# Kernel tuning notes

Hardware: AMD Instinct MI355X
Metric: run time of the kernel (lower is better)

Reference implementation:

```python
import jax, jax.numpy as jnp
import numpy as np

D_MODEL = 1024
H = 16
DK = D_MODEL // H


def setup_inputs() -> dict:
    key = jax.random.key(0)
    ks = jax.random.split(key, 13)
    B, S = 2, 2048
    scale = 1.0 / np.sqrt(D_MODEL)
    inp = {
        "query": jax.random.normal(ks[0], (B, S, D_MODEL), jnp.float32),
        "key": jax.random.normal(ks[1], (B, S, D_MODEL), jnp.float32),
        "value": jax.random.normal(ks[2], (B, S, D_MODEL), jnp.float32),
        "mask": jax.random.randint(ks[3], (B, 1, S, S), 0, 2, jnp.int32),
        "Wq": jax.random.normal(ks[4], (D_MODEL, D_MODEL), jnp.float32) * scale,
        "bq": jnp.zeros((D_MODEL,), jnp.float32),
        "Wk": jax.random.normal(ks[5], (D_MODEL, D_MODEL), jnp.float32) * scale,
        "bk": jnp.zeros((D_MODEL,), jnp.float32),
        "Wv": jax.random.normal(ks[6], (D_MODEL, D_MODEL), jnp.float32) * scale,
        "bv": jnp.zeros((D_MODEL,), jnp.float32),
        "Wo": jax.random.normal(ks[7], (D_MODEL, D_MODEL), jnp.float32) * scale,
        "bo": jnp.zeros((D_MODEL,), jnp.float32),
    }
    return inp


def _split_heads(x, W, b):
    # torch Linear: x @ W.T + b; then [B,S,D] -> [B,H,S,DK]
    B, S, _ = x.shape
    out = x @ W.T + b
    return out.reshape(B, S, H, DK).transpose(0, 2, 1, 3)


def reference(query, key, value, mask, Wq, bq, Wk, bk, Wv, bv, Wo, bo):
    B, S, _ = query.shape
    q = _split_heads(query, Wq, bq)   # [B,H,S,DK]
    k = _split_heads(key, Wk, bk)
    v = _split_heads(value, Wv, bv)
    scores = jnp.einsum("bhqd,bhkd->bhqk", q, k) / jnp.sqrt(jnp.asarray(DK, q.dtype))
    scores = jnp.where(mask == 0, jnp.asarray(-1e9, scores.dtype), scores)
    prob = jax.nn.softmax(scores, axis=-1)
    out = jnp.einsum("bhqk,bhkd->bhqd", prob, v)  # [B,H,S,DK]
    out = out.transpose(0, 2, 1, 3).reshape(B, S, D_MODEL)
    return out @ Wo.T + bo
```

## Files before the change

kernel.cpp:

```cpp
#include <hip/hip_runtime.h>
#include <hip/hip_bf16.h>

#define B_   2
#define S_   2048
#define DM   1024
#define NH   16
#define DKH  64
#define Mdim 4096
#define Ndim 1024
#define Kdim 1024

typedef __attribute__((ext_vector_type(8))) short bf16x8;
typedef __attribute__((ext_vector_type(4))) short bf16x4;
typedef __attribute__((ext_vector_type(4))) float f32x4;

__device__ __forceinline__ short f2b(float x) {
  union { __hip_bfloat16 h; short s; } u;
  u.h = __float2bfloat16(x);
  return u.s;
}

__device__ __forceinline__ void async_copy16(const void* g, void* l) {
  __builtin_amdgcn_global_load_lds(
      (const __attribute__((address_space(1))) unsigned int*)g,
      (__attribute__((address_space(3))) unsigned int*)l, 16, 0, 0);
}

struct Cvt7 {
  const float* src[7];
  ushort* dst[7];
  int n[7];
};

__global__ __launch_bounds__(256) void cvt_all(Cvt7 c) {
  const int ten = blockIdx.y;
  const int base = (blockIdx.x * 256 + threadIdx.x) * 8;
  if (base >= c.n[ten]) return;
  const float* s = c.src[ten] + base;
  float4 a = *(const float4*)s;
  float4 b = *(const float4*)(s + 4);
  bf16x8 r;
  r[0] = f2b(a.x); r[1] = f2b(a.y); r[2] = f2b(a.z); r[3] = f2b(a.w);
  r[4] = f2b(b.x); r[5] = f2b(b.y); r[6] = f2b(b.z); r[7] = f2b(b.w);
  *(bf16x8*)(c.dst[ten] + base) = r;
}

__device__ __forceinline__ void gstore(float* C, size_t i, float v) { C[i] = v; }
__device__ __forceinline__ void gstore(ushort* C, size_t i, float v) { C[i] = (ushort)f2b(v); }

template <typename OutT, int VT>
__global__ __launch_bounds__(256) void gemm128(const ushort* __restrict__ A,
                                               const ushort* __restrict__ W,
                                               const float* __restrict__ bias,
                                               OutT* __restrict__ C, float scale) {
  const int t = threadIdx.x;
  const int w = t >> 6, lane = t & 63;
  const int quad = lane >> 4, r16 = lane & 15;
  const int wr = w >> 1, wc = w & 1;
  const int row0 = blockIdx.x * 128, col0 = blockIdx.y * 64;

  __shared__ alignas(16) ushort a_s[128 * 32];
  __shared__ alignas(16) ushort b_s[64 * 32];

  const int sr = lane >> 2, sc = (lane & 3) * 8;
  const ushort* Ag0 = A + (size_t)(row0 + w * 32 + sr) * Kdim + sc;
  const ushort* Ag1 = Ag0 + (size_t)16 * Kdim;
  const ushort* Wg  = W + (size_t)(col0 + w * 16 + sr) * Kdim + sc;
  ushort* al0 = &a_s[(w * 32) * 32];
  ushort* al1 = &a_s[(w * 32 + 16) * 32];
  ushort* bl  = &b_s[(w * 16) * 32];

  f32x4 acc[4][2];
#pragma unroll
  for (int mt = 0; mt < 4; ++mt)
#pragma unroll
    for (int nt = 0; nt < 2; ++nt) acc[mt][nt] = (f32x4){0.f, 0.f, 0.f, 0.f};

  for (int k0 = 0; k0 < Kdim; k0 += 32) {
    __syncthreads();
    async_copy16(Ag0 + k0, al0);
    async_copy16(Ag1 + k0, al1);
    async_copy16(Wg + k0, bl);
    __syncthreads();

    bf16x8 af[4], bfr[2];
#pragma unroll
    for (int mt = 0; mt < 4; ++mt)
      af[mt] = *(const bf16x8*)&a_s[(wr * 64 + mt * 16 + r16) * 32 + quad * 8];
#pragma unroll
    for (int nt = 0; nt < 2; ++nt)
      bfr[nt] = *(const bf16x8*)&b_s[(wc * 32 + nt * 16 + r16) * 32 + quad * 8];
#pragma unroll
    for (int mt = 0; mt < 4; ++mt)
#pragma unroll
      for (int nt = 0; nt < 2; ++nt)
        acc[mt][nt] = __builtin_amdgcn_mfma_f32_16x16x32_bf16(af[mt], bfr[nt],
                                                              acc[mt][nt], 0, 0, 0);
  }

#pragma unroll
  for (int mt = 0; mt < 4; ++mt) {
#pragma unroll
    for (int nt = 0; nt < 2; ++nt) {
      const int col = col0 + wc * 32 + nt * 16 + r16;
      const float bv = bias[col];
      const int rowb = row0 + wr * 64 + mt * 16 + quad * 4;
#pragma unroll
      for (int i = 0; i < 4; ++i) {
        const float v = (acc[mt][nt][i] + bv) * scale;
        if (VT) {
          const int row = rowb + i;
          const int bb = row >> 11, ss = row & (S_ - 1);
          const int hh = col >> 6, dd = col & 63;
          gstore(C, (((size_t)bb * NH + hh) * 64 + dd) * S_ + ss, v);
        } else {
          gstore(C, (size_t)rowb * Ndim + (size_t)i * Ndim + col, v);
        }
      }
    }
  }
}

__global__ __launch_bounds__(256) void attn_mfma(const ushort* __restrict__ Qp,
                                                 const ushort* __restrict__ Kp,
                                                 const ushort* __restrict__ Vt,
                                                 const int* __restrict__ mask,
                                                 ushort* __restrict__ Oa) {
  const int bh = blockIdx.y;
  const int b = bh >> 4, h = bh & 15;
  const int q0 = blockIdx.x * 64;
  const int t = threadIdx.x;
  const int w = t >> 6, lane = t & 63, quad = lane >> 4, r16 = lane & 15;
  const size_t rb = (size_t)b * S_;

  __shared__ alignas(16) ushort k_s[64 * 64];
  __shared__ alignas(16) ushort vt_s[64 * 64];
  __shared__ alignas(16) ushort p_s[4][16 * 76];

  const ushort* qptr = Qp + (rb + q0 + w * 16 + r16) * DM + h * 64 + quad * 8;
  const bf16x8 aq0 = *(const bf16x8*)qptr;
  const bf16x8 aq1 = *(const bf16x8*)(qptr + 32);

  float l_i[4] = {0.f, 0.f, 0.f, 0.f};
  f32x4 oacc[4];
#pragma unroll
  for (int nt = 0; nt < 4; ++nt) oacc[nt] = (f32x4){0.f, 0.f, 0.f, 0.f};

  const int srow = t >> 3, schunk = t & 7;
  const ushort* kbase = Kp + (rb + srow) * DM + h * 64 + schunk * 8;
  const ushort* vbase = Vt + ((size_t)bh * 64 + srow) * S_ + schunk * 8;
  const int srow2 = srow + 32;

  for (int kt = 0; kt < S_; kt += 64) {
    __syncthreads();
    *(bf16x8*)&k_s[srow * 64 + ((schunk ^ (srow & 7)) * 8)] =
        *(const bf16x8*)(kbase + (size_t)kt * DM);
    *(bf16x8*)&k_s[srow2 * 64 + ((schunk ^ (srow2 & 7)) * 8)] =
        *(const bf16x8*)(kbase + (size_t)(kt + 32) * DM);
    *(bf16x8*)&vt_s[srow * 64 + ((schunk ^ (srow & 7)) * 8)] =
        *(const bf16x8*)(vbase + kt);
    *(bf16x8*)&vt_s[srow2 * 64 + ((schunk ^ (srow2 & 7)) * 8)] =
        *(const bf16x8*)(vbase + (size_t)32 * S_ + kt);
    __syncthreads();

    f32x4 sacc[4];
#pragma unroll
    for (int nt = 0; nt < 4; ++nt) {
      sacc[nt] = (f32x4){0.f, 0.f, 0.f, 0.f};
      const int krow = nt * 16 + r16;
      const bf16x8 b0 = *(const bf16x8*)&k_s[krow * 64 + ((quad ^ (krow & 7)) * 8)];
      const bf16x8 b1 = *(const bf16x8*)&k_s[krow * 64 + (((4 + quad) ^ (krow & 7)) * 8)];
      sacc[nt] = __builtin_amdgcn_mfma_f32_16x16x32_bf16(aq0, b0, sacc[nt], 0, 0, 0);
      sacc[nt] = __builtin_amdgcn_mfma_f32_16x16x32_bf16(aq1, b1, sacc[nt], 0, 0, 0);
    }

    const int* mrow = mask + (size_t)b * S_ * S_ +
                      (size_t)(q0 + w * 16 + quad * 4) * S_ + kt;
#pragma unroll
    for (int i = 0; i < 4; ++i) {
      float ps = 0.f;
#pragma unroll
      for (int nt = 0; nt < 4; ++nt) {
        const int mv = mrow[(size_t)i * S_ + nt * 16 + r16];
        const float p = (mv == 0) ? 0.f : __expf(sacc[nt][i]);
        ps += p;
        p_s[w][(quad * 4 + i) * 76 + nt * 16 + r16] = (ushort)f2b(p);
      }
      l_i[i] += ps;
    }

#pragma unroll
    for (int ks = 0; ks < 2; ++ks) {
      const bf16x4 lo = *(const bf16x4*)&p_s[w][r16 * 76 + ks * 32 + quad * 8];
      const bf16x4 hi = *(const bf16x4*)&p_s[w][r16 * 76 + ks * 32 + quad * 8 + 4];
      bf16x8 pa;
#pragma unroll
      for (int j = 0; j < 4; ++j) { pa[j] = lo[j]; pa[4 + j] = hi[j]; }
      const int kc = ks * 4 + quad;
#pragma unroll
      for (int nt = 0; nt < 4; ++nt) {
        const int dk = nt * 16 + r16;
        const bf16x8 vb = *(const bf16x8*)&vt_s[dk * 64 + ((kc ^ (dk & 7)) * 8)];
        oacc[nt] = __builtin_amdgcn_mfma_f32_16x16x32_bf16(pa, vb, oacc[nt], 0, 0, 0);
      }
    }
  }

#pragma unroll
  for (int i = 0; i < 4; ++i) {
    float l = l_i[i];
#pragma unroll
    for (int off = 1; off < 16; off <<= 1) l += __shfl_xor(l, off);
    l_i[i] = l;
  }
#pragma unroll
  for (int nt = 0; nt < 4; ++nt) {
#pragma unroll
    for (int i = 0; i < 4; ++i) {
      const int row = q0 + w * 16 + quad * 4 + i;
      const int col = h * 64 + nt * 16 + r16;
      Oa[(rb + row) * DM + col] = (ushort)f2b(oacc[nt][i] / l_i[i]);
    }
  }
}

extern "C" void kernel_launch(void* const* d_in, const int* in_sizes, int n_in,
                              void* d_out, int out_size, void* d_ws, size_t ws_size,
                              hipStream_t stream) {
  const int* mask = (const int*)d_in[3];
  const float* bq = (const float*)d_in[5];
  const float* bk = (const float*)d_in[7];
  const float* bv = (const float*)d_in[9];
  const float* bo = (const float*)d_in[11];

  const size_t NE = (size_t)B_ * S_ * DM;
  const size_t NW = (size_t)DM * DM;

  ushort* qc = (ushort*)d_ws;
  ushort* kc = qc + NE;
  ushort* vc = kc + NE;
  ushort* Qp = vc + NE;
  ushort* Kp = Qp + NE;
  ushort* Vt = Kp + NE;
  ushort* Wqc = Vt + NE;
  ushort* Wkc = Wqc + NW;
  ushort* Wvc = Wkc + NW;
  ushort* Woc = Wvc + NW;

  Cvt7 c;
  const int sidx[7] = {0, 1, 2, 4, 6, 8, 10};
  ushort* dsts[7] = {qc, kc, vc, Wqc, Wkc, Wvc, Woc};
  for (int i = 0; i < 7; ++i) {
    c.src[i] = (const float*)d_in[sidx[i]];
    c.dst[i] = dsts[i];
    c.n[i] = (i < 3) ? (int)NE : (int)NW;
  }
  cvt_all<<<dim3(2048, 7), 256, 0, stream>>>(c);

  dim3 gg(Mdim / 128, Ndim / 64);
  gemm128<ushort, 0><<<gg, 256, 0, stream>>>(qc, Wqc, bq, Qp, 0.125f);
  gemm128<ushort, 0><<<gg, 256, 0, stream>>>(kc, Wkc, bk, Kp, 1.0f);
  gemm128<ushort, 1><<<gg, 256, 0, stream>>>(vc, Wvc, bv, Vt, 1.0f);

  attn_mfma<<<dim3(S_ / 64, B_ * NH), 256, 0, stream>>>(Qp, Kp, Vt, mask, qc);

  gemm128<float, 0><<<gg, 256, 0, stream>>>(qc, Woc, bo, (float*)d_out, 1.0f);
}
```

Baseline: 291.9 us.

## Pack mask to bitmask, pre-swizzle K/V layouts for async LDS loads, widen GEMM tiles

Adds a kernel that packs the int32 mask into 64-bit ballot bitmasks, so attention reads far fewer mask bytes. The K and V projection GEMMs now write head-major, XOR-swizzled layouts, which lets attention stage K/V tiles with direct global-to-LDS async copies instead of register round trips. GEMM tiles grow from 128x64 to 128x128 to increase reuse. The packed mask is stored in the kc buffer after the K projection has consumed it, which relies on stream ordering.

```diff
diff --git a/kernel.cpp b/kernel.cpp
--- a/kernel.cpp
+++ b/kernel.cpp
@@ -5,9 +5,7 @@
 #define S_   2048
 #define DM   1024
 #define NH   16
-#define DKH  64
 #define Mdim 4096
-#define Ndim 1024
 #define Kdim 1024
 
 typedef __attribute__((ext_vector_type(8))) short bf16x8;
@@ -45,55 +43,64 @@
   *(bf16x8*)(c.dst[ten] + base) = r;
 }
 
-__device__ __forceinline__ void gstore(float* C, size_t i, float v) { C[i] = v; }
-__device__ __forceinline__ void gstore(ushort* C, size_t i, float v) { C[i] = (ushort)f2b(v); }
-
-template <typename OutT, int VT>
-__global__ __launch_bounds__(256) void gemm128(const ushort* __restrict__ A,
-                                               const ushort* __restrict__ W,
-                                               const float* __restrict__ bias,
-                                               OutT* __restrict__ C, float scale) {
+__global__ __launch_bounds__(256) void pack_mask(const int* __restrict__ mask,
+                                                 unsigned long long* __restrict__ mpk) {
+  const int gw = (blockIdx.x * 256 + threadIdx.x) >> 6;
+  const int lane = threadIdx.x & 63;
+  const int mv = mask[(size_t)gw * 64 + lane];
+  const unsigned long long bits = __ballot(mv != 0);
+  if (lane == 0) mpk[gw] = bits;
+}
+
+template <int MODE>
+__global__ __launch_bounds__(256) void gemm_m97(const ushort* __restrict__ A,
+                                                const ushort* __restrict__ W,
+                                                const float* __restrict__ bias,
+                                                void* __restrict__ Cv, float scale) {
   const int t = threadIdx.x;
   const int w = t >> 6, lane = t & 63;
   const int quad = lane >> 4, r16 = lane & 15;
   const int wr = w >> 1, wc = w & 1;
-  const int row0 = blockIdx.x * 128, col0 = blockIdx.y * 64;
+  const int row0 = blockIdx.x * 128, col0 = blockIdx.y * 128;
 
   __shared__ alignas(16) ushort a_s[128 * 32];
-  __shared__ alignas(16) ushort b_s[64 * 32];
-
-  const int sr = lane >> 2, sc = (lane & 3) * 8;
-  const ushort* Ag0 = A + (size_t)(row0 + w * 32 + sr) * Kdim + sc;
-  const ushort* Ag1 = Ag0 + (size_t)16 * Kdim;
-  const ushort* Wg  = W + (size_t)(col0 + w * 16 + sr) * Kdim + sc;
-  ushort* al0 = &a_s[(w * 32) * 32];
-  ushort* al1 = &a_s[(w * 32 + 16) * 32];
-  ushort* bl  = &b_s[(w * 16) * 32];
-
-  f32x4 acc[4][2];
+  __shared__ alignas(16) ushort b_s[128 * 32];
+
+  const int sr = t >> 2, sc = (t & 3) * 8;
+  const ushort* Ag0 = A + (size_t)(row0 + sr) * Kdim + sc;
+  const ushort* Ag1 = Ag0 + (size_t)64 * Kdim;
+  const ushort* Wg0 = W + (size_t)(col0 + sr) * Kdim + sc;
+  const ushort* Wg1 = Wg0 + (size_t)64 * Kdim;
+  ushort* al0 = &a_s[w * 512];
+  ushort* al1 = &a_s[2048 + w * 512];
+  ushort* bl0 = &b_s[w * 512];
+  ushort* bl1 = &b_s[2048 + w * 512];
+
+  f32x4 acc[4][4];
 #pragma unroll
   for (int mt = 0; mt < 4; ++mt)
 #pragma unroll
-    for (int nt = 0; nt < 2; ++nt) acc[mt][nt] = (f32x4){0.f, 0.f, 0.f, 0.f};
+    for (int nt = 0; nt < 4; ++nt) acc[mt][nt] = (f32x4){0.f, 0.f, 0.f, 0.f};
 
   for (int k0 = 0; k0 < Kdim; k0 += 32) {
     __syncthreads();
     async_copy16(Ag0 + k0, al0);
     async_copy16(Ag1 + k0, al1);
-    async_copy16(Wg + k0, bl);
-    __syncthreads();
-
-    bf16x8 af[4], bfr[2];
+    async_copy16(Wg0 + k0, bl0);
+    async_copy16(Wg1 + k0, bl1);
+    __syncthreads();
+
+    bf16x8 af[4], bfr[4];
 #pragma unroll
     for (int mt = 0; mt < 4; ++mt)
       af[mt] = *(const bf16x8*)&a_s[(wr * 64 + mt * 16 + r16) * 32 + quad * 8];
 #pragma unroll
-    for (int nt = 0; nt < 2; ++nt)
-      bfr[nt] = *(const bf16x8*)&b_s[(wc * 32 + nt * 16 + r16) * 32 + quad * 8];
+    for (int nt = 0; nt < 4; ++nt)
+      bfr[nt] = *(const bf16x8*)&b_s[(wc * 64 + nt * 16 + r16) * 32 + quad * 8];
 #pragma unroll
     for (int mt = 0; mt < 4; ++mt)
 #pragma unroll
-      for (int nt = 0; nt < 2; ++nt)
+      for (int nt = 0; nt < 4; ++nt)
         acc[mt][nt] = __builtin_amdgcn_mfma_f32_16x16x32_bf16(af[mt], bfr[nt],
                                                               acc[mt][nt], 0, 0, 0);
   }
@@ -101,20 +108,30 @@
 #pragma unroll
   for (int mt = 0; mt < 4; ++mt) {
 #pragma unroll
-    for (int nt = 0; nt < 2; ++nt) {
-      const int col = col0 + wc * 32 + nt * 16 + r16;
+    for (int nt = 0; nt < 4; ++nt) {
+      const int col = col0 + wc * 64 + nt * 16 + r16;
       const float bv = bias[col];
       const int rowb = row0 + wr * 64 + mt * 16 + quad * 4;
 #pragma unroll
       for (int i = 0; i < 4; ++i) {
         const float v = (acc[mt][nt][i] + bv) * scale;
-        if (VT) {
-          const int row = rowb + i;
-          const int bb = row >> 11, ss = row & (S_ - 1);
-          const int hh = col >> 6, dd = col & 63;
-          gstore(C, (((size_t)bb * NH + hh) * 64 + dd) * S_ + ss, v);
+        const int row = rowb + i;
+        if (MODE == 0) {
+          ((float*)Cv)[(size_t)row * DM + col] = v;
+        } else if (MODE == 1) {
+          ((ushort*)Cv)[(size_t)row * DM + col] = (ushort)f2b(v);
+        } else if (MODE == 2) {
+          const int bb = row >> 11, s = row & (S_ - 1);
+          const int hh = col >> 6, d = col & 63;
+          const size_t idx = ((size_t)(bb * NH + hh) * S_ + s) * 64 +
+                             (((d >> 3) ^ (s & 7)) * 8) + (d & 7);
+          ((ushort*)Cv)[idx] = (ushort)f2b(v);
         } else {
-          gstore(C, (size_t)rowb * Ndim + (size_t)i * Ndim + col, v);
+          const int bb = row >> 11, s = row & (S_ - 1);
+          const int hh = col >> 6, d = col & 63;
+          const size_t idx = ((size_t)(bb * NH + hh) * 64 + d) * S_ + (s & ~63) +
+                             ((((s >> 3) & 7) ^ (d & 7)) * 8) + (s & 7);
+          ((ushort*)Cv)[idx] = (ushort)f2b(v);
         }
       }
     }
@@ -122,9 +139,9 @@
 }
 
 __global__ __launch_bounds__(256) void attn_mfma(const ushort* __restrict__ Qp,
-                                                 const ushort* __restrict__ Kp,
-                                                 const ushort* __restrict__ Vt,
-                                                 const int* __restrict__ mask,
+                                                 const ushort* __restrict__ Kg,
+                                                 const ushort* __restrict__ Vg,
+                                                 const unsigned long long* __restrict__ mpk,
                                                  ushort* __restrict__ Oa) {
   const int bh = blockIdx.y;
   const int b = bh >> 4, h = bh & 15;
@@ -147,20 +164,21 @@
   for (int nt = 0; nt < 4; ++nt) oacc[nt] = (f32x4){0.f, 0.f, 0.f, 0.f};
 
   const int srow = t >> 3, schunk = t & 7;
-  const ushort* kbase = Kp + (rb + srow) * DM + h * 64 + schunk * 8;
-  const ushort* vbase = Vt + ((size_t)bh * 64 + srow) * S_ + schunk * 8;
-  const int srow2 = srow + 32;
+  const ushort* kgb = Kg + ((size_t)bh * S_ + srow) * 64 + schunk * 8;
+  const ushort* vgb = Vg + ((size_t)bh * 64 + srow) * S_ + schunk * 8;
+  ushort* kl0 = &k_s[w * 512];
+  ushort* kl1 = &k_s[2048 + w * 512];
+  ushort* vl0 = &vt_s[w * 512];
+  ushort* vl1 = &vt_s[2048 + w * 512];
+
+  const unsigned long long* mrowp = mpk + (rb + q0 + w * 16 + quad * 4) * 32;
 
   for (int kt = 0; kt < S_; kt += 64) {
     __syncthreads();
-    *(bf16x8*)&k_s[srow * 64 + ((schunk ^ (srow & 7)) * 8)] =
-        *(const bf16x8*)(kbase + (size_t)kt * DM);
-    *(bf16x8*)&k_s[srow2 * 64 + ((schunk ^ (srow2 & 7)) * 8)] =
-        *(const bf16x8*)(kbase + (size_t)(kt + 32) * DM);
-    *(bf16x8*)&vt_s[srow * 64 + ((schunk ^ (srow & 7)) * 8)] =
-        *(const bf16x8*)(vbase + kt);
-    *(bf16x8*)&vt_s[srow2 * 64 + ((schunk ^ (srow2 & 7)) * 8)] =
-        *(const bf16x8*)(vbase + (size_t)32 * S_ + kt);
+    async_copy16(kgb + (size_t)kt * 64, kl0);
+    async_copy16(kgb + (size_t)(kt + 32) * 64, kl1);
+    async_copy16(vgb + kt, vl0);
+    async_copy16(vgb + (size_t)32 * S_ + kt, vl1);
     __syncthreads();
 
     f32x4 sacc[4];
@@ -174,15 +192,15 @@
       sacc[nt] = __builtin_amdgcn_mfma_f32_16x16x32_bf16(aq1, b1, sacc[nt], 0, 0, 0);
     }
 
-    const int* mrow = mask + (size_t)b * S_ * S_ +
-                      (size_t)(q0 + w * 16 + quad * 4) * S_ + kt;
+    const int seg = kt >> 6;
 #pragma unroll
     for (int i = 0; i < 4; ++i) {
+      const unsigned long long mbits = mrowp[i * 32 + seg];
       float ps = 0.f;
 #pragma unroll
       for (int nt = 0; nt < 4; ++nt) {
-        const int mv = mrow[(size_t)i * S_ + nt * 16 + r16];
-        const float p = (mv == 0) ? 0.f : __expf(sacc[nt][i]);
+        const unsigned int bit = (unsigned int)(mbits >> (nt * 16 + r16)) & 1u;
+        const float p = bit ? __expf(sacc[nt][i]) : 0.f;
         ps += p;
         p_s[w][(quad * 4 + i) * 76 + nt * 16 + r16] = (ushort)f2b(p);
       }
@@ -240,12 +258,13 @@
   ushort* kc = qc + NE;
   ushort* vc = kc + NE;
   ushort* Qp = vc + NE;
-  ushort* Kp = Qp + NE;
-  ushort* Vt = Kp + NE;
-  ushort* Wqc = Vt + NE;
+  ushort* Kg = Qp + NE;
+  ushort* Vg = Kg + NE;
+  ushort* Wqc = Vg + NE;
   ushort* Wkc = Wqc + NW;
   ushort* Wvc = Wkc + NW;
   ushort* Woc = Wvc + NW;
+  unsigned long long* mpk = (unsigned long long*)kc;
 
   Cvt7 c;
   const int sidx[7] = {0, 1, 2, 4, 6, 8, 10};
@@ -257,12 +276,14 @@
   }
   cvt_all<<<dim3(2048, 7), 256, 0, stream>>>(c);
 
-  dim3 gg(Mdim / 128, Ndim / 64);
-  gemm128<ushort, 0><<<gg, 256, 0, stream>>>(qc, Wqc, bq, Qp, 0.125f);
-  gemm128<ushort, 0><<<gg, 256, 0, stream>>>(kc, Wkc, bk, Kp, 1.0f);
-  gemm128<ushort, 1><<<gg, 256, 0, stream>>>(vc, Wvc, bv, Vt, 1.0f);
-
-  attn_mfma<<<dim3(S_ / 64, B_ * NH), 256, 0, stream>>>(Qp, Kp, Vt, mask, qc);
-
-  gemm128<float, 0><<<gg, 256, 0, stream>>>(qc, Woc, bo, (float*)d_out, 1.0f);
-}
+  dim3 gg(Mdim / 128, DM / 128);
+  gemm_m97<1><<<gg, 256, 0, stream>>>(qc, Wqc, bq, Qp, 0.125f);
+  gemm_m97<2><<<gg, 256, 0, stream>>>(kc, Wkc, bk, Kg, 1.0f);
+  gemm_m97<3><<<gg, 256, 0, stream>>>(vc, Wvc, bv, Vg, 1.0f);
+
+  pack_mask<<<(B_ * S_ * (S_ / 64) * 64) / 256, 256, 0, stream>>>(mask, mpk);
+
+  attn_mfma<<<dim3(S_ / 64, B_ * NH), 256, 0, stream>>>(Qp, Kg, Vg, mpk, qc);
+
+  gemm_m97<0><<<gg, 256, 0, stream>>>(qc, Woc, bo, (float*)d_out, 1.0f);
+}
```

After: 314.4 us. +7.7%, slower.
